# Optimization experiments

Measured on AMD Instinct MI355X. Metric: run time of the kernel, lower is better.

## Reference

```python
import jax, jax.numpy as jnp
import numpy as np

NUM_EXPERTS = 8
D_MODEL = 1024
HIDDEN = 3 * D_MODEL
TOP_K = 2
LAMBDA = 0.01


def setup_inputs() -> dict:
    key = jax.random.key(0)
    k_x, k_w1, k_w2, k_r = jax.random.split(key, 4)
    B, T, C = 4, 2048, D_MODEL
    x = jax.random.normal(k_x, (B, T, C), dtype=jnp.float32)
    # per-expert SwishFFN weights (bias=False): W1 [E, C, H], W2 [E, H, C]
    W1 = jax.random.normal(k_w1, (NUM_EXPERTS, C, HIDDEN), dtype=jnp.float32) * (1.0 / np.sqrt(C))
    W2 = jax.random.normal(k_w2, (NUM_EXPERTS, HIDDEN, C), dtype=jnp.float32) * (1.0 / np.sqrt(HIDDEN))
    # router projection [C, E]
    Wr = jax.random.normal(k_r, (C, NUM_EXPERTS), dtype=jnp.float32) * (1.0 / np.sqrt(C))
    return {"x": x, "W1": W1, "W2": W2, "Wr": Wr}


def reference(x, W1, W2, Wr):
    B, T, C = x.shape
    E = W1.shape[0]
    xf = x.reshape(-1, C)                       # [N, C], N = B*T
    N = xf.shape[0]

    # Router: softmax over experts, keep top-k, renormalize among the k
    logits = xf @ Wr                            # [N, E]
    all_probs = jax.nn.softmax(logits, axis=-1)
    vals, idx = jax.lax.top_k(all_probs, TOP_K)  # [N, K]
    vals = vals / jnp.sum(vals, axis=-1, keepdims=True)
    routing_weight = jnp.zeros((N, E), dtype=xf.dtype).at[
        jnp.arange(N)[:, None], idx
    ].set(vals)                                  # sparse [N, E]

    # Expert combine: sum_e w_e * FFN_e(x); w_e == 0 for non-selected tokens,
    # so this equals the original masked gather/scatter loop exactly.
    out = jnp.zeros_like(xf)
    for e in range(E):
        h = jax.nn.silu(xf @ W1[e])              # [N, H]
        out = out + routing_weight[:, e:e + 1] * (h @ W2[e])

    # Load-balancing aux loss (fi detached)
    fi = jax.lax.stop_gradient(
        jnp.mean((routing_weight > 0).astype(xf.dtype), axis=0))
    pi = jnp.mean(all_probs, axis=0)
    aux_loss = LAMBDA * E * jnp.sum(fi * pi)

    return out.reshape(B, T, C), aux_loss
```

## Files before the change

### kernel.cpp

```cpp
#include <hip/hip_runtime.h>
#include <stdint.h>

#define N_TOK 8192
#define C_DIM 1024
#define H_DIM 3072
#define N_EXP 8
#define N_ASSIGN (N_TOK * 2)

typedef __attribute__((ext_vector_type(8))) short short8;
typedef __attribute__((ext_vector_type(4))) float f32x4;

__device__ __forceinline__ unsigned short f2bf(float f) {
    union { float f; uint32_t u; } v; v.f = f;
    uint32_t r = (v.u + 0x7FFFu + ((v.u >> 16) & 1u)) >> 16;
    return (unsigned short)r;
}

#define GLDS16(SRC, DST) __builtin_amdgcn_global_load_lds( \
    (const __attribute__((address_space(1))) void*)(SRC),  \
    (__attribute__((address_space(3))) void*)(DST), 16, 0, 0)

__global__ __launch_bounds__(256) void transpose_bf16_kernel(const float* __restrict__ in,
                                                             unsigned short* __restrict__ out,
                                                             int rows, int cols) {
    __shared__ float tile[64][65];
    int e = blockIdx.z;
    const float* ip = in + (size_t)e * rows * cols;
    unsigned short* op = out + (size_t)e * rows * cols;
    int c0 = blockIdx.x * 64;
    int r0 = blockIdx.y * 64;
    int t = threadIdx.x;
    int lr = t >> 4, lc4 = t & 15;
#pragma unroll
    for (int it = 0; it < 4; it++) {
        int r = lr + it * 16;
        float4 v = *(const float4*)&ip[(size_t)(r0 + r) * cols + c0 + lc4 * 4];
        tile[lc4 * 4 + 0][r] = v.x;
        tile[lc4 * 4 + 1][r] = v.y;
        tile[lc4 * 4 + 2][r] = v.z;
        tile[lc4 * 4 + 3][r] = v.w;
    }
    __syncthreads();
#pragma unroll
    for (int it = 0; it < 4; it++) {
        int oc = lr + it * 16;
        ushort4 o;
        o.x = f2bf(tile[oc][lc4 * 4 + 0]);
        o.y = f2bf(tile[oc][lc4 * 4 + 1]);
        o.z = f2bf(tile[oc][lc4 * 4 + 2]);
        o.w = f2bf(tile[oc][lc4 * 4 + 3]);
        *(ushort4*)&op[(size_t)(c0 + oc) * rows + r0 + lc4 * 4] = o;
    }
}

__global__ __launch_bounds__(256) void router_kernel(const float* __restrict__ x, const float* __restrict__ Wr,
                                                     int2* __restrict__ idx2, float2* __restrict__ wgt2,
                                                     float* __restrict__ piAcc, int* __restrict__ cntAcc) {
    __shared__ float s_pi[8];
    __shared__ int s_cnt[8];
    int t = threadIdx.x;
    if (t < 8) { s_pi[t] = 0.f; s_cnt[t] = 0; }
    __syncthreads();
    int lane = t & 63;
    int wid = t >> 6;
    int gwv = blockIdx.x * 4 + wid;
    int nw = gridDim.x * 4;
    for (int n = gwv; n < N_TOK; n += nw) {
        float acc[8];
#pragma unroll
        for (int e = 0; e < 8; e++) acc[e] = 0.f;
        const float* xr = x + (size_t)n * C_DIM;
#pragma unroll
        for (int j = 0; j < 16; j++) {
            int k = lane + 64 * j;
            float xv = xr[k];
            const float4* wr4 = (const float4*)(Wr + (size_t)k * 8);
            float4 a = wr4[0], b = wr4[1];
            acc[0] += xv * a.x; acc[1] += xv * a.y; acc[2] += xv * a.z; acc[3] += xv * a.w;
            acc[4] += xv * b.x; acc[5] += xv * b.y; acc[6] += xv * b.z; acc[7] += xv * b.w;
        }
#pragma unroll
        for (int off = 1; off < 64; off <<= 1) {
#pragma unroll
            for (int e = 0; e < 8; e++) acc[e] += __shfl_xor(acc[e], off, 64);
        }
        float m = acc[0];
#pragma unroll
        for (int e = 1; e < 8; e++) m = fmaxf(m, acc[e]);
        float p[8]; float s = 0.f;
#pragma unroll
        for (int e = 0; e < 8; e++) { p[e] = __expf(acc[e] - m); s += p[e]; }
        float inv = 1.f / s;
#pragma unroll
        for (int e = 0; e < 8; e++) p[e] *= inv;
        int i0 = 0; float l0 = acc[0];
#pragma unroll
        for (int e = 1; e < 8; e++) if (acc[e] > l0) { l0 = acc[e]; i0 = e; }
        int i1 = -1; float l1 = -1e30f;
#pragma unroll
        for (int e = 0; e < 8; e++) if (e != i0 && acc[e] > l1) { l1 = acc[e]; i1 = e; }
        if (lane == 0) {
            float v0 = p[i0], v1 = p[i1];
            float rs = 1.f / (v0 + v1);
            idx2[n] = make_int2(i0, i1);
            wgt2[n] = make_float2(v0 * rs, v1 * rs);
            atomicAdd(&s_cnt[i0], 1);
            atomicAdd(&s_cnt[i1], 1);
#pragma unroll
            for (int e = 0; e < 8; e++) atomicAdd(&s_pi[e], p[e]);
        }
    }
    __syncthreads();
    if (t < 8) { atomicAdd(&piAcc[t], s_pi[t]); atomicAdd(&cntAcc[t], s_cnt[t]); }
}

__global__ void finalize_router_kernel(const int* __restrict__ cnt, const float* __restrict__ pi,
                                       int* __restrict__ off, float* __restrict__ aux_out) {
    if (threadIdx.x == 0) {
        int o = 0;
        float dot = 0.f;
        for (int e = 0; e < 8; e++) {
            off[e] = o;
            o += cnt[e];
            dot += (float)cnt[e] * pi[e];
        }
        aux_out[0] = 0.01f * 8.f * dot / ((float)N_TOK * (float)N_TOK);
    }
}

__global__ __launch_bounds__(256) void scatter_kernel(const int2* __restrict__ idx2, const float2* __restrict__ wgt2,
                                                      const int* __restrict__ off, int* __restrict__ cursor,
                                                      int* __restrict__ tok, float* __restrict__ gwArr) {
    __shared__ int lcnt[8], lbase[8];
    int t = threadIdx.x;
    if (t < 8) lcnt[t] = 0;
    __syncthreads();
    int a = blockIdx.x * 256 + t;
    int n = a >> 1, k = a & 1;
    int2 id = idx2[n];
    float2 w = wgt2[n];
    int e = k ? id.y : id.x;
    float wv = k ? w.y : w.x;
    int rank = atomicAdd(&lcnt[e], 1);
    __syncthreads();
    if (t < 8) lbase[t] = atomicAdd(&cursor[t], lcnt[t]);
    __syncthreads();
    int pos = off[e] + lbase[e] + rank;
    tok[pos] = n;
    gwArr[pos] = wv;
}

__global__ __launch_bounds__(256) void gather_kernel(const float* __restrict__ x, const int* __restrict__ tok,
                                                     unsigned short* __restrict__ xg) {
    int wid = threadIdx.x >> 6, lane = threadIdx.x & 63;
    int row = blockIdx.x * 4 + wid;
    int n = tok[row];
    const float4* src = (const float4*)(x + (size_t)n * C_DIM);
    ushort4* dst = (ushort4*)(xg + (size_t)row * C_DIM);
#pragma unroll
    for (int j = 0; j < 4; j++) {
        float4 v = src[lane + 64 * j];
        ushort4 o;
        o.x = f2bf(v.x); o.y = f2bf(v.y); o.z = f2bf(v.z); o.w = f2bf(v.w);
        dst[lane + 64 * j] = o;
    }
}

template <int EPI>
__global__ __launch_bounds__(256) void moe_gemm_kernel(
    const unsigned short* __restrict__ A, int ldA,
    const unsigned short* __restrict__ Bt, int ldB, int bRowOff, int bColOff,
    int Kseg, int NY, int SK,
    const int* __restrict__ cnt, const int* __restrict__ off,
    const int* __restrict__ tok, const float* __restrict__ gwArr,
    unsigned short* __restrict__ hs, int ldH,
    float* __restrict__ out) {
    __shared__ unsigned short As[8192];
    __shared__ unsigned short Bs[8192];

    int nbs[8];
    int tot = 0;
#pragma unroll
    for (int i = 0; i < 8; i++) {
        nbs[i] = (cnt[i] + 127) >> 7;
        tot += nbs[i] * NY * SK;
    }
    int p = blockIdx.x;
    int q = tot >> 3, r = tot & 7;
    int xx = p & 7, sp = p >> 3;
    int capx = (xx < r) ? q + 1 : q;
    if (sp >= capx) return;
    int wi = (xx < r) ? xx * (q + 1) + sp : r * (q + 1) + (xx - r) * q + sp;

    int base = 0, e = -1, enb = 0, local = 0;
#pragma unroll
    for (int i = 0; i < 8; i++) {
        int sz = nbs[i] * NY * SK;
        if (e < 0 && wi < base + sz) { e = i; enb = nbs[i]; local = wi - base; }
        base += sz;
    }
    if (e < 0) return;
    int ys = local / enb;
    int mblk = local - ys * enb;
    int s = ys / NY;
    int y = ys - s * NY;
    int M = cnt[e];
    int m0 = mblk * 128;
    int baseRow = off[e];
    int n0 = y * 128;
    int acol = s * Kseg;
    int bcol = bColOff + s * Kseg;

    int tid = threadIdx.x;
    int lane = tid & 63;
    int wid = tid >> 6;
    int wm = (wid >> 1) * 64;
    int wn = (wid & 1) * 64;

    f32x4 acc[4][4];
#pragma unroll
    for (int i = 0; i < 4; i++)
#pragma unroll
        for (int j = 0; j < 4; j++) acc[i][j] = (f32x4)0.f;

    const unsigned short* Bex = Bt + (size_t)e * (size_t)(C_DIM * H_DIM);

    const unsigned short* srcA[4];
    const unsigned short* srcB[4];
    int ldsOff[4];
#pragma unroll
    for (int i = 0; i < 4; i++) {
        int c = i * 256 + tid;
        int row = c >> 3;
        int pos = c & 7;
        int sc = pos ^ (row & 7);
        int rg = m0 + row; if (rg > M - 1) rg = M - 1;
        srcA[i] = A + (size_t)(baseRow + rg) * ldA + acol + sc * 8;
        srcB[i] = Bex + (size_t)(bRowOff + n0 + row) * ldB + bcol + sc * 8;
        ldsOff[i] = (c & ~63) * 8;
    }

    int kq = lane >> 4;
    int rsub = lane & 15;
    int offAr[2][4], offBr[2][4];
#pragma unroll
    for (int kk = 0; kk < 2; kk++) {
#pragma unroll
        for (int m = 0; m < 4; m++) {
            int rr = wm + m * 16 + rsub;
            offAr[kk][m] = rr * 64 + (((kk * 4 + kq) ^ (rr & 7)) * 8);
        }
#pragma unroll
        for (int n = 0; n < 4; n++) {
            int rn = wn + n * 16 + rsub;
            offBr[kk][n] = rn * 64 + (((kk * 4 + kq) ^ (rn & 7)) * 8);
        }
    }

    int nt = Kseg >> 6;
#pragma unroll 1
    for (int t = 0; t < nt; ++t) {
#pragma unroll
        for (int i = 0; i < 4; i++) {
            GLDS16(srcA[i], &As[ldsOff[i]]);
            GLDS16(srcB[i], &Bs[ldsOff[i]]);
            srcA[i] += 64; srcB[i] += 64;
        }
        __syncthreads();
#pragma unroll
        for (int kk = 0; kk < 2; kk++) {
            short8 a[4], b[4];
#pragma unroll
            for (int m = 0; m < 4; m++) a[m] = *(const short8*)&As[offAr[kk][m]];
#pragma unroll
            for (int n = 0; n < 4; n++) b[n] = *(const short8*)&Bs[offBr[kk][n]];
#pragma unroll
            for (int m = 0; m < 4; m++)
#pragma unroll
                for (int n = 0; n < 4; n++)
                    acc[m][n] = __builtin_amdgcn_mfma_f32_16x16x32_bf16(a[m], b[n], acc[m][n], 0, 0, 0);
        }
        __syncthreads();
    }

    int gRow = (lane >> 4) * 4;
    int cLane = lane & 15;
#pragma unroll
    for (int m = 0; m < 4; m++) {
#pragma unroll
        for (int j = 0; j < 4; j++) {
            int rr = m0 + wm + m * 16 + gRow + j;
            if (rr < M) {
                if (EPI == 0) {
#pragma unroll
                    for (int n = 0; n < 4; n++) {
                        int c = n0 + wn + n * 16 + cLane;
                        float v = acc[m][n][j];
                        float sv = v / (1.f + __expf(-v));
                        hs[(size_t)(baseRow + rr) * ldH + c] = f2bf(sv);
                    }
                } else {
                    int token = tok[baseRow + rr];
                    float w = gwArr[baseRow + rr];
#pragma unroll
                    for (int n = 0; n < 4; n++) {
                        int c = n0 + wn + n * 16 + cLane;
                        atomicAdd(&out[(size_t)token * C_DIM + c], w * acc[m][n][j]);
                    }
                }
            }
        }
    }
}

extern "C" void kernel_launch(void* const* d_in, const int* in_sizes, int n_in,
                              void* d_out, int out_size, void* d_ws, size_t ws_size,
                              hipStream_t stream) {
    const float* x = (const float*)d_in[0];
    const float* W1 = (const float*)d_in[1];
    const float* W2 = (const float*)d_in[2];
    const float* Wr = (const float*)d_in[3];
    float* out = (float*)d_out;

    char* p = (char*)d_ws;
    auto alloc = [&](size_t bytes) {
        char* r = p;
        p += (bytes + 255) & ~(size_t)255;
        return r;
    };
    float* pi = (float*)alloc(8 * sizeof(float));
    int* cntA = (int*)alloc(8 * sizeof(int));
    int* cursor = (int*)alloc(8 * sizeof(int));
    int* offA = (int*)alloc(8 * sizeof(int));
    int2* idx2 = (int2*)alloc((size_t)N_TOK * sizeof(int2));
    float2* wgt2 = (float2*)alloc((size_t)N_TOK * sizeof(float2));
    int* tok = (int*)alloc((size_t)N_ASSIGN * sizeof(int));
    float* gwA = (float*)alloc((size_t)N_ASSIGN * sizeof(float));
    unsigned short* W1bT = (unsigned short*)alloc((size_t)N_EXP * C_DIM * H_DIM * 2);
    unsigned short* W2bT = (unsigned short*)alloc((size_t)N_EXP * C_DIM * H_DIM * 2);
    unsigned short* xg = (unsigned short*)alloc((size_t)N_ASSIGN * C_DIM * 2);
    size_t used = (size_t)(p - (char*)d_ws);
    size_t remain = ws_size > used ? ws_size - used : 0;
    int HC = H_DIM;
    while (HC > 384 && (size_t)N_ASSIGN * HC * 2 > remain) HC >>= 1;
    unsigned short* hs = (unsigned short*)p;

    hipMemsetAsync(d_ws, 0, 1024, stream);
    hipMemsetAsync(d_out, 0, (size_t)N_TOK * C_DIM * sizeof(float), stream);

    transpose_bf16_kernel<<<dim3(H_DIM / 64, C_DIM / 64, N_EXP), 256, 0, stream>>>(W1, W1bT, C_DIM, H_DIM);
    transpose_bf16_kernel<<<dim3(C_DIM / 64, H_DIM / 64, N_EXP), 256, 0, stream>>>(W2, W2bT, H_DIM, C_DIM);

    router_kernel<<<256, 256, 0, stream>>>(x, Wr, idx2, wgt2, pi, cntA);
    finalize_router_kernel<<<1, 64, 0, stream>>>(cntA, pi, offA, out + (size_t)N_TOK * C_DIM);
    scatter_kernel<<<N_ASSIGN / 256, 256, 0, stream>>>(idx2, wgt2, offA, cursor, tok, gwA);
    gather_kernel<<<N_ASSIGN / 4, 256, 0, stream>>>(x, tok, xg);

    int nChunks = H_DIM / HC;
    for (int ci = 0; ci < nChunks; ++ci) {
        int h0 = ci * HC;
        int ny1 = HC / 128;
        int sk2 = (HC >= 1536) ? 2 : 1;
        moe_gemm_kernel<0><<<dim3(135 * ny1 + 8, 1, 1), 256, 0, stream>>>(
            xg, C_DIM, W1bT, C_DIM, h0, 0, C_DIM, ny1, 1,
            cntA, offA, tok, gwA, hs, HC, out);
        moe_gemm_kernel<1><<<dim3(135 * 8 * sk2 + 8, 1, 1), 256, 0, stream>>>(
            hs, HC, W2bT, H_DIM, 0, h0, HC / sk2, 8, sk2,
            cntA, offA, tok, gwA, hs, HC, out);
    }
}
```

Baseline: 450.9 us.

## Use 256x256 tiles with 4-stage async LDS pipeline in MoE GEMM

```diff
diff --git a/kernel.cpp b/kernel.cpp
--- a/kernel.cpp
+++ b/kernel.cpp
@@ -19,6 +19,14 @@
 #define GLDS16(SRC, DST) __builtin_amdgcn_global_load_lds( \
     (const __attribute__((address_space(1))) void*)(SRC),  \
     (__attribute__((address_space(3))) void*)(DST), 16, 0, 0)
+
+#define SBAR() do { __builtin_amdgcn_sched_barrier(0); \
+    __builtin_amdgcn_s_barrier();                      \
+    __builtin_amdgcn_sched_barrier(0); } while (0)
+
+#define VM_WAIT(S) do { __builtin_amdgcn_sched_barrier(0); \
+    asm volatile(S ::: "memory");                          \
+    __builtin_amdgcn_sched_barrier(0); } while (0)
 
 __global__ __launch_bounds__(256) void transpose_bf16_kernel(const float* __restrict__ in,
                                                              unsigned short* __restrict__ out,
@@ -167,7 +175,7 @@
 }
 
 template <int EPI>
-__global__ __launch_bounds__(256) void moe_gemm_kernel(
+__global__ __launch_bounds__(512) void moe_gemm_kernel(
     const unsigned short* __restrict__ A, int ldA,
     const unsigned short* __restrict__ Bt, int ldB, int bRowOff, int bColOff,
     int Kseg, int NY, int SK,
@@ -175,14 +183,13 @@
     const int* __restrict__ tok, const float* __restrict__ gwArr,
     unsigned short* __restrict__ hs, int ldH,
     float* __restrict__ out) {
-    __shared__ unsigned short As[8192];
-    __shared__ unsigned short Bs[8192];
+    __shared__ unsigned short smem[65536];
 
     int nbs[8];
     int tot = 0;
 #pragma unroll
     for (int i = 0; i < 8; i++) {
-        nbs[i] = (cnt[i] + 127) >> 7;
+        nbs[i] = (cnt[i] + 255) >> 8;
         tot += nbs[i] * NY * SK;
     }
     int p = blockIdx.x;
@@ -205,35 +212,35 @@
     int s = ys / NY;
     int y = ys - s * NY;
     int M = cnt[e];
-    int m0 = mblk * 128;
+    int m0 = mblk * 256;
     int baseRow = off[e];
-    int n0 = y * 128;
+    int n0 = y * 256;
     int acol = s * Kseg;
     int bcol = bColOff + s * Kseg;
 
     int tid = threadIdx.x;
     int lane = tid & 63;
     int wid = tid >> 6;
-    int wm = (wid >> 1) * 64;
-    int wn = (wid & 1) * 64;
-
-    f32x4 acc[4][4];
-#pragma unroll
-    for (int i = 0; i < 4; i++)
+    int wm = (wid >> 2) * 128;
+    int wn = (wid & 3) * 64;
+
+    f32x4 acc[8][4];
+#pragma unroll
+    for (int i = 0; i < 8; i++)
 #pragma unroll
         for (int j = 0; j < 4; j++) acc[i][j] = (f32x4)0.f;
 
     const unsigned short* Bex = Bt + (size_t)e * (size_t)(C_DIM * H_DIM);
 
-    const unsigned short* srcA[4];
-    const unsigned short* srcB[4];
-    int ldsOff[4];
-#pragma unroll
-    for (int i = 0; i < 4; i++) {
-        int c = i * 256 + tid;
-        int row = c >> 3;
-        int pos = c & 7;
-        int sc = pos ^ (row & 7);
+    const unsigned short* srcA[2];
+    const unsigned short* srcB[2];
+    int ldsOff[2];
+#pragma unroll
+    for (int i = 0; i < 2; i++) {
+        int c = i * 512 + tid;
+        int row = c >> 2;
+        int pos = c & 3;
+        int sc = pos ^ ((row >> 1) & 3);
         int rg = m0 + row; if (rg > M - 1) rg = M - 1;
         srcA[i] = A + (size_t)(baseRow + rg) * ldA + acol + sc * 8;
         srcB[i] = Bex + (size_t)(bRowOff + n0 + row) * ldB + bcol + sc * 8;
@@ -242,51 +249,63 @@
 
     int kq = lane >> 4;
     int rsub = lane & 15;
-    int offAr[2][4], offBr[2][4];
-#pragma unroll
-    for (int kk = 0; kk < 2; kk++) {
-#pragma unroll
-        for (int m = 0; m < 4; m++) {
-            int rr = wm + m * 16 + rsub;
-            offAr[kk][m] = rr * 64 + (((kk * 4 + kq) ^ (rr & 7)) * 8);
-        }
-#pragma unroll
-        for (int n = 0; n < 4; n++) {
-            int rn = wn + n * 16 + rsub;
-            offBr[kk][n] = rn * 64 + (((kk * 4 + kq) ^ (rn & 7)) * 8);
-        }
-    }
-
-    int nt = Kseg >> 6;
+    int offA[8], offB[4];
+#pragma unroll
+    for (int m = 0; m < 8; m++) {
+        int rr = wm + m * 16 + rsub;
+        offA[m] = rr * 32 + ((kq ^ ((rr >> 1) & 3)) * 8);
+    }
+#pragma unroll
+    for (int n = 0; n < 4; n++) {
+        int rn = wn + n * 16 + rsub;
+        offB[n] = 8192 + rn * 32 + ((kq ^ ((rn >> 1) & 3)) * 8);
+    }
+
+    int nt = Kseg >> 5;
+#pragma unroll
+    for (int tt = 0; tt < 3; tt++) {
+#pragma unroll
+        for (int i = 0; i < 2; i++) GLDS16(srcA[i], &smem[tt * 16384 + ldsOff[i]]);
+#pragma unroll
+        for (int i = 0; i < 2; i++) GLDS16(srcB[i], &smem[tt * 16384 + 8192 + ldsOff[i]]);
+#pragma unroll
+        for (int i = 0; i < 2; i++) { srcA[i] += 32; srcB[i] += 32; }
+    }
+
 #pragma unroll 1
     for (int t = 0; t < nt; ++t) {
-#pragma unroll
-        for (int i = 0; i < 4; i++) {
-            GLDS16(srcA[i], &As[ldsOff[i]]);
-            GLDS16(srcB[i], &Bs[ldsOff[i]]);
-            srcA[i] += 64; srcB[i] += 64;
-        }
-        __syncthreads();
-#pragma unroll
-        for (int kk = 0; kk < 2; kk++) {
-            short8 a[4], b[4];
-#pragma unroll
-            for (int m = 0; m < 4; m++) a[m] = *(const short8*)&As[offAr[kk][m]];
-#pragma unroll
-            for (int n = 0; n < 4; n++) b[n] = *(const short8*)&Bs[offBr[kk][n]];
-#pragma unroll
-            for (int m = 0; m < 4; m++)
-#pragma unroll
-                for (int n = 0; n < 4; n++)
-                    acc[m][n] = __builtin_amdgcn_mfma_f32_16x16x32_bf16(a[m], b[n], acc[m][n], 0, 0, 0);
-        }
-        __syncthreads();
+        if (t < nt - 2)      VM_WAIT("s_waitcnt vmcnt(8)");
+        else if (t == nt - 2) VM_WAIT("s_waitcnt vmcnt(4)");
+        else                 VM_WAIT("s_waitcnt vmcnt(0)");
+        SBAR();
+        const unsigned short* buf = &smem[(t & 3) * 16384];
+        short8 a[8], b[4];
+#pragma unroll
+        for (int m = 0; m < 8; m++) a[m] = *(const short8*)&buf[offA[m]];
+#pragma unroll
+        for (int n = 0; n < 4; n++) b[n] = *(const short8*)&buf[offB[n]];
+        if (t + 3 < nt) {
+            int bb = ((t + 3) & 3) * 16384;
+#pragma unroll
+            for (int i = 0; i < 2; i++) GLDS16(srcA[i], &smem[bb + ldsOff[i]]);
+#pragma unroll
+            for (int i = 0; i < 2; i++) GLDS16(srcB[i], &smem[bb + 8192 + ldsOff[i]]);
+#pragma unroll
+            for (int i = 0; i < 2; i++) { srcA[i] += 32; srcB[i] += 32; }
+        }
+        __builtin_amdgcn_s_setprio(1);
+#pragma unroll
+        for (int m = 0; m < 8; m++)
+#pragma unroll
+            for (int n = 0; n < 4; n++)
+                acc[m][n] = __builtin_amdgcn_mfma_f32_16x16x32_bf16(a[m], b[n], acc[m][n], 0, 0, 0);
+        __builtin_amdgcn_s_setprio(0);
     }
 
     int gRow = (lane >> 4) * 4;
     int cLane = lane & 15;
 #pragma unroll
-    for (int m = 0; m < 4; m++) {
+    for (int m = 0; m < 8; m++) {
 #pragma unroll
         for (int j = 0; j < 4; j++) {
             int rr = m0 + wm + m * 16 + gRow + j;
@@ -342,7 +361,7 @@
     size_t used = (size_t)(p - (char*)d_ws);
     size_t remain = ws_size > used ? ws_size - used : 0;
     int HC = H_DIM;
-    while (HC > 384 && (size_t)N_ASSIGN * HC * 2 > remain) HC >>= 1;
+    while (HC > 768 && (size_t)N_ASSIGN * HC * 2 > remain) HC >>= 1;
     unsigned short* hs = (unsigned short*)p;
 
     hipMemsetAsync(d_ws, 0, 1024, stream);
@@ -359,13 +378,13 @@
     int nChunks = H_DIM / HC;
     for (int ci = 0; ci < nChunks; ++ci) {
         int h0 = ci * HC;
-        int ny1 = HC / 128;
-        int sk2 = (HC >= 1536) ? 2 : 1;
-        moe_gemm_kernel<0><<<dim3(135 * ny1 + 8, 1, 1), 256, 0, stream>>>(
+        int ny1 = HC / 256;
+        int sk2 = (HC % 768 == 0) ? 3 : 2;
+        moe_gemm_kernel<0><<<dim3(71 * ny1 + 8, 1, 1), 512, 0, stream>>>(
             xg, C_DIM, W1bT, C_DIM, h0, 0, C_DIM, ny1, 1,
             cntA, offA, tok, gwA, hs, HC, out);
-        moe_gemm_kernel<1><<<dim3(135 * 8 * sk2 + 8, 1, 1), 256, 0, stream>>>(
-            hs, HC, W2bT, H_DIM, 0, h0, HC / sk2, 8, sk2,
+        moe_gemm_kernel<1><<<dim3(71 * 4 * sk2 + 8, 1, 1), 512, 0, stream>>>(
+            hs, HC, W2bT, H_DIM, 0, h0, HC / sk2, 4, sk2,
             cntA, offA, tok, gwA, hs, HC, out);
     }
 }
```

Result: slower. 506.7 us (+12.4%).

## Double-buffer GEMM LDS tiles with K=32 steps and merge weight transposes

Applied to the files above, without the earlier changes.

```diff
diff --git a/kernel.cpp b/kernel.cpp
--- a/kernel.cpp
+++ b/kernel.cpp
@@ -20,15 +20,34 @@
     (const __attribute__((address_space(1))) void*)(SRC),  \
     (__attribute__((address_space(3))) void*)(DST), 16, 0, 0)
 
-__global__ __launch_bounds__(256) void transpose_bf16_kernel(const float* __restrict__ in,
-                                                             unsigned short* __restrict__ out,
-                                                             int rows, int cols) {
+#define SBAR() do { __builtin_amdgcn_sched_barrier(0); \
+    __builtin_amdgcn_s_barrier();                      \
+    __builtin_amdgcn_sched_barrier(0); } while (0)
+
+#define VM_WAIT(S) do { __builtin_amdgcn_sched_barrier(0); \
+    asm volatile(S ::: "memory");                          \
+    __builtin_amdgcn_sched_barrier(0); } while (0)
+
+__global__ __launch_bounds__(256) void transpose_both_kernel(const float* __restrict__ W1,
+                                                             const float* __restrict__ W2,
+                                                             unsigned short* __restrict__ o1,
+                                                             unsigned short* __restrict__ o2) {
     __shared__ float tile[64][65];
-    int e = blockIdx.z;
-    const float* ip = in + (size_t)e * rows * cols;
-    unsigned short* op = out + (size_t)e * rows * cols;
-    int c0 = blockIdx.x * 64;
-    int r0 = blockIdx.y * 64;
+    int z = blockIdx.z;
+    const float* ip;
+    unsigned short* op;
+    int rows, cols, c0, r0;
+    if (z < 8) {
+        ip = W1 + (size_t)z * C_DIM * H_DIM;
+        op = o1 + (size_t)z * C_DIM * H_DIM;
+        rows = C_DIM; cols = H_DIM;
+        c0 = blockIdx.x * 64; r0 = blockIdx.y * 64;
+    } else {
+        ip = W2 + (size_t)(z - 8) * C_DIM * H_DIM;
+        op = o2 + (size_t)(z - 8) * C_DIM * H_DIM;
+        rows = H_DIM; cols = C_DIM;
+        c0 = blockIdx.y * 64; r0 = blockIdx.x * 64;
+    }
     int t = threadIdx.x;
     int lr = t >> 4, lc4 = t & 15;
 #pragma unroll
@@ -175,8 +194,8 @@
     const int* __restrict__ tok, const float* __restrict__ gwArr,
     unsigned short* __restrict__ hs, int ldH,
     float* __restrict__ out) {
-    __shared__ unsigned short As[8192];
-    __shared__ unsigned short Bs[8192];
+    __shared__ unsigned short As[2][4096];
+    __shared__ unsigned short Bs[2][4096];
 
     int nbs[8];
     int tot = 0;
@@ -225,15 +244,15 @@
 
     const unsigned short* Bex = Bt + (size_t)e * (size_t)(C_DIM * H_DIM);
 
-    const unsigned short* srcA[4];
-    const unsigned short* srcB[4];
-    int ldsOff[4];
-#pragma unroll
-    for (int i = 0; i < 4; i++) {
+    const unsigned short* srcA[2];
+    const unsigned short* srcB[2];
+    int ldsOff[2];
+#pragma unroll
+    for (int i = 0; i < 2; i++) {
         int c = i * 256 + tid;
-        int row = c >> 3;
-        int pos = c & 7;
-        int sc = pos ^ (row & 7);
+        int row = c >> 2;
+        int pos = c & 3;
+        int sc = pos ^ ((row >> 1) & 3);
         int rg = m0 + row; if (rg > M - 1) rg = M - 1;
         srcA[i] = A + (size_t)(baseRow + rg) * ldA + acol + sc * 8;
         srcB[i] = Bex + (size_t)(bRowOff + n0 + row) * ldB + bcol + sc * 8;
@@ -242,45 +261,55 @@
 
     int kq = lane >> 4;
     int rsub = lane & 15;
-    int offAr[2][4], offBr[2][4];
-#pragma unroll
-    for (int kk = 0; kk < 2; kk++) {
-#pragma unroll
-        for (int m = 0; m < 4; m++) {
-            int rr = wm + m * 16 + rsub;
-            offAr[kk][m] = rr * 64 + (((kk * 4 + kq) ^ (rr & 7)) * 8);
-        }
-#pragma unroll
-        for (int n = 0; n < 4; n++) {
-            int rn = wn + n * 16 + rsub;
-            offBr[kk][n] = rn * 64 + (((kk * 4 + kq) ^ (rn & 7)) * 8);
-        }
-    }
-
-    int nt = Kseg >> 6;
+    int offA[4], offB[4];
+#pragma unroll
+    for (int m = 0; m < 4; m++) {
+        int rr = wm + m * 16 + rsub;
+        offA[m] = rr * 32 + ((kq ^ ((rr >> 1) & 3)) * 8);
+    }
+#pragma unroll
+    for (int n = 0; n < 4; n++) {
+        int rn = wn + n * 16 + rsub;
+        offB[n] = rn * 32 + ((kq ^ ((rn >> 1) & 3)) * 8);
+    }
+
+    int nt = Kseg >> 5;
+#pragma unroll
+    for (int i = 0; i < 2; i++) GLDS16(srcA[i], &As[0][ldsOff[i]]);
+#pragma unroll
+    for (int i = 0; i < 2; i++) GLDS16(srcB[i], &Bs[0][ldsOff[i]]);
+#pragma unroll
+    for (int i = 0; i < 2; i++) { srcA[i] += 32; srcB[i] += 32; }
+
 #pragma unroll 1
     for (int t = 0; t < nt; ++t) {
-#pragma unroll
-        for (int i = 0; i < 4; i++) {
-            GLDS16(srcA[i], &As[ldsOff[i]]);
-            GLDS16(srcB[i], &Bs[ldsOff[i]]);
-            srcA[i] += 64; srcB[i] += 64;
-        }
-        __syncthreads();
-#pragma unroll
-        for (int kk = 0; kk < 2; kk++) {
-            short8 a[4], b[4];
-#pragma unroll
-            for (int m = 0; m < 4; m++) a[m] = *(const short8*)&As[offAr[kk][m]];
-#pragma unroll
-            for (int n = 0; n < 4; n++) b[n] = *(const short8*)&Bs[offBr[kk][n]];
-#pragma unroll
-            for (int m = 0; m < 4; m++)
-#pragma unroll
-                for (int n = 0; n < 4; n++)
-                    acc[m][n] = __builtin_amdgcn_mfma_f32_16x16x32_bf16(a[m], b[n], acc[m][n], 0, 0, 0);
-        }
-        __syncthreads();
+        if (t + 1 < nt) {
+            int nb = (t + 1) & 1;
+#pragma unroll
+            for (int i = 0; i < 2; i++) GLDS16(srcA[i], &As[nb][ldsOff[i]]);
+#pragma unroll
+            for (int i = 0; i < 2; i++) GLDS16(srcB[i], &Bs[nb][ldsOff[i]]);
+#pragma unroll
+            for (int i = 0; i < 2; i++) { srcA[i] += 32; srcB[i] += 32; }
+            VM_WAIT("s_waitcnt vmcnt(4)");
+        } else {
+            VM_WAIT("s_waitcnt vmcnt(0)");
+        }
+        SBAR();
+        int cb = t & 1;
+        short8 a[4], b[4];
+#pragma unroll
+        for (int m = 0; m < 4; m++) a[m] = *(const short8*)&As[cb][offA[m]];
+#pragma unroll
+        for (int n = 0; n < 4; n++) b[n] = *(const short8*)&Bs[cb][offB[n]];
+        __builtin_amdgcn_s_setprio(1);
+#pragma unroll
+        for (int m = 0; m < 4; m++)
+#pragma unroll
+            for (int n = 0; n < 4; n++)
+                acc[m][n] = __builtin_amdgcn_mfma_f32_16x16x32_bf16(a[m], b[n], acc[m][n], 0, 0, 0);
+        __builtin_amdgcn_s_setprio(0);
+        SBAR();
     }
 
     int gRow = (lane >> 4) * 4;
@@ -348,8 +377,7 @@
     hipMemsetAsync(d_ws, 0, 1024, stream);
     hipMemsetAsync(d_out, 0, (size_t)N_TOK * C_DIM * sizeof(float), stream);
 
-    transpose_bf16_kernel<<<dim3(H_DIM / 64, C_DIM / 64, N_EXP), 256, 0, stream>>>(W1, W1bT, C_DIM, H_DIM);
-    transpose_bf16_kernel<<<dim3(C_DIM / 64, H_DIM / 64, N_EXP), 256, 0, stream>>>(W2, W2bT, H_DIM, C_DIM);
+    transpose_both_kernel<<<dim3(48, 16, 16), 256, 0, stream>>>(W1, W2, W1bT, W2bT);
 
     router_kernel<<<256, 256, 0, stream>>>(x, Wr, idx2, wgt2, pi, cntA);
     finalize_router_kernel<<<1, 64, 0, stream>>>(cntA, pi, offA, out + (size_t)N_TOK * C_DIM);
```

Result: slower. 476.6 us (+5.7%).

## Widen MoE GEMM tiles to 128x256 and fuse weight transposes into one launch

Applied to the files above, without the earlier changes.

```diff
diff --git a/kernel.cpp b/kernel.cpp
--- a/kernel.cpp
+++ b/kernel.cpp
@@ -20,15 +20,26 @@
     (const __attribute__((address_space(1))) void*)(SRC),  \
     (__attribute__((address_space(3))) void*)(DST), 16, 0, 0)
 
-__global__ __launch_bounds__(256) void transpose_bf16_kernel(const float* __restrict__ in,
-                                                             unsigned short* __restrict__ out,
-                                                             int rows, int cols) {
+__global__ __launch_bounds__(256) void transpose_both_kernel(const float* __restrict__ W1,
+                                                             const float* __restrict__ W2,
+                                                             unsigned short* __restrict__ o1,
+                                                             unsigned short* __restrict__ o2) {
     __shared__ float tile[64][65];
-    int e = blockIdx.z;
-    const float* ip = in + (size_t)e * rows * cols;
-    unsigned short* op = out + (size_t)e * rows * cols;
-    int c0 = blockIdx.x * 64;
-    int r0 = blockIdx.y * 64;
+    int z = blockIdx.z;
+    const float* ip;
+    unsigned short* op;
+    int rows, cols, c0, r0;
+    if (z < 8) {
+        ip = W1 + (size_t)z * C_DIM * H_DIM;
+        op = o1 + (size_t)z * C_DIM * H_DIM;
+        rows = C_DIM; cols = H_DIM;
+        c0 = blockIdx.x * 64; r0 = blockIdx.y * 64;
+    } else {
+        ip = W2 + (size_t)(z - 8) * C_DIM * H_DIM;
+        op = o2 + (size_t)(z - 8) * C_DIM * H_DIM;
+        rows = H_DIM; cols = C_DIM;
+        c0 = blockIdx.y * 64; r0 = blockIdx.x * 64;
+    }
     int t = threadIdx.x;
     int lr = t >> 4, lc4 = t & 15;
 #pragma unroll
@@ -176,7 +187,7 @@
     unsigned short* __restrict__ hs, int ldH,
     float* __restrict__ out) {
     __shared__ unsigned short As[8192];
-    __shared__ unsigned short Bs[8192];
+    __shared__ unsigned short Bs[16384];
 
     int nbs[8];
     int tot = 0;
@@ -207,7 +218,7 @@
     int M = cnt[e];
     int m0 = mblk * 128;
     int baseRow = off[e];
-    int n0 = y * 128;
+    int n0 = y * 256;
     int acol = s * Kseg;
     int bcol = bColOff + s * Kseg;
 
@@ -215,34 +226,40 @@
     int lane = tid & 63;
     int wid = tid >> 6;
     int wm = (wid >> 1) * 64;
-    int wn = (wid & 1) * 64;
-
-    f32x4 acc[4][4];
+    int wn = (wid & 1) * 128;
+
+    f32x4 acc[4][8];
 #pragma unroll
     for (int i = 0; i < 4; i++)
 #pragma unroll
-        for (int j = 0; j < 4; j++) acc[i][j] = (f32x4)0.f;
+        for (int j = 0; j < 8; j++) acc[i][j] = (f32x4)0.f;
 
     const unsigned short* Bex = Bt + (size_t)e * (size_t)(C_DIM * H_DIM);
 
     const unsigned short* srcA[4];
-    const unsigned short* srcB[4];
-    int ldsOff[4];
+    const unsigned short* srcB[8];
+    int ldsA[4], ldsB[8];
 #pragma unroll
     for (int i = 0; i < 4; i++) {
         int c = i * 256 + tid;
         int row = c >> 3;
-        int pos = c & 7;
-        int sc = pos ^ (row & 7);
+        int sc = (c & 7) ^ (row & 7);
         int rg = m0 + row; if (rg > M - 1) rg = M - 1;
         srcA[i] = A + (size_t)(baseRow + rg) * ldA + acol + sc * 8;
+        ldsA[i] = (c & ~63) * 8;
+    }
+#pragma unroll
+    for (int i = 0; i < 8; i++) {
+        int c = i * 256 + tid;
+        int row = c >> 3;
+        int sc = (c & 7) ^ (row & 7);
         srcB[i] = Bex + (size_t)(bRowOff + n0 + row) * ldB + bcol + sc * 8;
-        ldsOff[i] = (c & ~63) * 8;
+        ldsB[i] = (c & ~63) * 8;
     }
 
     int kq = lane >> 4;
     int rsub = lane & 15;
-    int offAr[2][4], offBr[2][4];
+    int offAr[2][4], offBr[2][8];
 #pragma unroll
     for (int kk = 0; kk < 2; kk++) {
 #pragma unroll
@@ -251,7 +268,7 @@
             offAr[kk][m] = rr * 64 + (((kk * 4 + kq) ^ (rr & 7)) * 8);
         }
 #pragma unroll
-        for (int n = 0; n < 4; n++) {
+        for (int n = 0; n < 8; n++) {
             int rn = wn + n * 16 + rsub;
             offBr[kk][n] = rn * 64 + (((kk * 4 + kq) ^ (rn & 7)) * 8);
         }
@@ -261,23 +278,21 @@
 #pragma unroll 1
     for (int t = 0; t < nt; ++t) {
 #pragma unroll
-        for (int i = 0; i < 4; i++) {
-            GLDS16(srcA[i], &As[ldsOff[i]]);
-            GLDS16(srcB[i], &Bs[ldsOff[i]]);
-            srcA[i] += 64; srcB[i] += 64;
-        }
+        for (int i = 0; i < 4; i++) { GLDS16(srcA[i], &As[ldsA[i]]); srcA[i] += 64; }
+#pragma unroll
+        for (int i = 0; i < 8; i++) { GLDS16(srcB[i], &Bs[ldsB[i]]); srcB[i] += 64; }
         __syncthreads();
 #pragma unroll
         for (int kk = 0; kk < 2; kk++) {
-            short8 a[4], b[4];
+            short8 a[4], b[8];
 #pragma unroll
             for (int m = 0; m < 4; m++) a[m] = *(const short8*)&As[offAr[kk][m]];
 #pragma unroll
-            for (int n = 0; n < 4; n++) b[n] = *(const short8*)&Bs[offBr[kk][n]];
+            for (int n = 0; n < 8; n++) b[n] = *(const short8*)&Bs[offBr[kk][n]];
 #pragma unroll
             for (int m = 0; m < 4; m++)
 #pragma unroll
-                for (int n = 0; n < 4; n++)
+                for (int n = 0; n < 8; n++)
                     acc[m][n] = __builtin_amdgcn_mfma_f32_16x16x32_bf16(a[m], b[n], acc[m][n], 0, 0, 0);
         }
         __syncthreads();
@@ -293,7 +308,7 @@
             if (rr < M) {
                 if (EPI == 0) {
 #pragma unroll
-                    for (int n = 0; n < 4; n++) {
+                    for (int n = 0; n < 8; n++) {
                         int c = n0 + wn + n * 16 + cLane;
                         float v = acc[m][n][j];
                         float sv = v / (1.f + __expf(-v));
@@ -303,7 +318,7 @@
                     int token = tok[baseRow + rr];
                     float w = gwArr[baseRow + rr];
 #pragma unroll
-                    for (int n = 0; n < 4; n++) {
+                    for (int n = 0; n < 8; n++) {
                         int c = n0 + wn + n * 16 + cLane;
                         atomicAdd(&out[(size_t)token * C_DIM + c], w * acc[m][n][j]);
                     }
@@ -342,14 +357,13 @@
     size_t used = (size_t)(p - (char*)d_ws);
     size_t remain = ws_size > used ? ws_size - used : 0;
     int HC = H_DIM;
-    while (HC > 384 && (size_t)N_ASSIGN * HC * 2 > remain) HC >>= 1;
+    while (HC > 768 && (size_t)N_ASSIGN * HC * 2 > remain) HC >>= 1;
     unsigned short* hs = (unsigned short*)p;
 
     hipMemsetAsync(d_ws, 0, 1024, stream);
     hipMemsetAsync(d_out, 0, (size_t)N_TOK * C_DIM * sizeof(float), stream);
 
-    transpose_bf16_kernel<<<dim3(H_DIM / 64, C_DIM / 64, N_EXP), 256, 0, stream>>>(W1, W1bT, C_DIM, H_DIM);
-    transpose_bf16_kernel<<<dim3(C_DIM / 64, H_DIM / 64, N_EXP), 256, 0, stream>>>(W2, W2bT, H_DIM, C_DIM);
+    transpose_both_kernel<<<dim3(48, 16, 16), 256, 0, stream>>>(W1, W2, W1bT, W2bT);
 
     router_kernel<<<256, 256, 0, stream>>>(x, Wr, idx2, wgt2, pi, cntA);
     finalize_router_kernel<<<1, 64, 0, stream>>>(cntA, pi, offA, out + (size_t)N_TOK * C_DIM);
@@ -359,13 +373,13 @@
     int nChunks = H_DIM / HC;
     for (int ci = 0; ci < nChunks; ++ci) {
         int h0 = ci * HC;
-        int ny1 = HC / 128;
-        int sk2 = (HC >= 1536) ? 2 : 1;
+        int ny1 = HC / 256;
+        int sk2 = 3;
         moe_gemm_kernel<0><<<dim3(135 * ny1 + 8, 1, 1), 256, 0, stream>>>(
             xg, C_DIM, W1bT, C_DIM, h0, 0, C_DIM, ny1, 1,
             cntA, offA, tok, gwA, hs, HC, out);
-        moe_gemm_kernel<1><<<dim3(135 * 8 * sk2 + 8, 1, 1), 256, 0, stream>>>(
-            hs, HC, W2bT, H_DIM, 0, h0, HC / sk2, 8, sk2,
+        moe_gemm_kernel<1><<<dim3(135 * 4 * sk2 + 8, 1, 1), 256, 0, stream>>>(
+            hs, HC, W2bT, H_DIM, 0, h0, HC / sk2, 4, sk2,
             cntA, offA, tok, gwA, hs, HC, out);
     }
 }
```

Measured after the change: 729.1 us. 61.7% more time.
